# Kernel tuning notes

Hardware: AMD Instinct MI355X
Metric: run time of the kernel (lower is better)

The kernel has to match this reference:

```python
import jax, jax.numpy as jnp
import numpy as np

B, T, C, H = 4, 1024, 1024, 16
D = C // H  # head_dim = 64


def _make_sin_cos(t, d, dtype=jnp.float32):
    # Standard RoPE tables: freqs = pos * inv_freq, emb = concat(freqs, freqs)
    inv_freq = 1.0 / (10000.0 ** (jnp.arange(0, d, 2, dtype=jnp.float32) / d))
    freqs = jnp.arange(t, dtype=jnp.float32)[:, None] * inv_freq[None, :]  # [T, D/2]
    emb = jnp.concatenate([freqs, freqs], axis=-1)  # [T, D]
    return jnp.sin(emb).astype(dtype), jnp.cos(emb).astype(dtype)


def setup_inputs() -> dict:
    key = jax.random.key(0)
    ks = jax.random.split(key, 6)
    sin, cos = _make_sin_cos(T, D)
    return {
        "x": jax.random.normal(ks[0], (B, T, C), jnp.float32),
        "qkv_w": jax.random.normal(ks[1], (3 * C, C), jnp.float32) * (C ** -0.5),
        "qkv_b": jax.random.normal(ks[2], (3 * C,), jnp.float32) * 0.02,
        "out_w": jax.random.normal(ks[3], (C, C), jnp.float32) * (C ** -0.5),
        "out_b": jax.random.normal(ks[4], (C,), jnp.float32) * 0.02,
        "rel_bias": jax.random.normal(ks[5], (H, T, T), jnp.float32) * 0.1,
        "sin": sin,
        "cos": cos,
        "head_gains": jnp.ones((H,), jnp.float32),
    }


def _rotate_half(u):
    u1, u2 = jnp.split(u, 2, axis=-1)
    return jnp.concatenate([-u2, u1], axis=-1)


def reference(x, qkv_w, qkv_b, out_w, out_b, rel_bias, sin, cos, head_gains):
    b, t, c = x.shape
    h, d = H, D
    scale = d ** -0.5
    # QKV projection: [B,T,3C] -> [3,B,H,T,D]
    qkv = (jnp.einsum("btc,oc->bto", x, qkv_w) + qkv_b).reshape(b, t, 3, h, d)
    qkv = jnp.transpose(qkv, (2, 0, 3, 1, 4))
    q, k, v = qkv[0], qkv[1], qkv[2]  # each [B,H,T,D]
    # RoPE
    s = sin[None, None]  # [1,1,T,D]
    co = cos[None, None]
    q = q * co + _rotate_half(q) * s
    k = k * co + _rotate_half(k) * s
    # Scores + additive relative-position bias (non-flash path)
    scores = jnp.einsum("bhtd,bhsd->bhts", q * scale, k) + rel_bias[None]
    attn = jax.nn.softmax(scores, axis=-1)  # dropout_p = 0 (eval)
    ctx = jnp.einsum("bhts,bhsd->bhtd", attn, v)
    ctx = ctx * head_gains[None, :, None, None]  # head-wise gain scaling
    merged = jnp.transpose(ctx, (0, 2, 1, 3)).reshape(b, t, c)
    out = jnp.einsum("btc,oc->bto", merged, out_w) + out_b
    return out, ctx, attn
```

## Files before the change

### kernel.cpp

```cpp
#include <hip/hip_runtime.h>
#include <stdint.h>

#define B_ 4
#define T_ 1024
#define C_ 1024
#define H_ 16
#define D_ 64

typedef __bf16 bf16x8 __attribute__((ext_vector_type(8)));
typedef short  s16x8  __attribute__((ext_vector_type(8)));
typedef short  s16x4  __attribute__((ext_vector_type(4)));
typedef float  f32x4  __attribute__((ext_vector_type(4)));
typedef float  f32x2  __attribute__((ext_vector_type(2)));

__device__ inline f32x4 mfma16(s16x8 a, s16x8 b, f32x4 c) {
    return __builtin_amdgcn_mfma_f32_16x16x32_bf16(a, b, c, 0, 0, 0);
}

__device__ inline void split_pack(f32x4 a, f32x4 b, s16x8& hi, s16x8& lo) {
    bf16x8 h, l;
    #pragma unroll
    for (int j = 0; j < 4; j++) {
        __bf16 x = (__bf16)a[j]; h[j]     = x; l[j]     = (__bf16)(a[j] - (float)x);
        __bf16 y = (__bf16)b[j]; h[j + 4] = y; l[j + 4] = (__bf16)(b[j] - (float)y);
    }
    hi = __builtin_bit_cast(s16x8, h);
    lo = __builtin_bit_cast(s16x8, l);
}

template<int MODE>
__global__ __launch_bounds__(256) void k_gemm_3p(const float* __restrict__ A,
                                                 const float* __restrict__ Bw,
                                                 const float* __restrict__ bias,
                                                 float* __restrict__ Cout,
                                                 int N, int K) {
    const int m0 = blockIdx.y * 128, n0 = blockIdx.x * 128;
    __shared__ __attribute__((aligned(16))) __bf16 Ah[128 * 40];
    __shared__ __attribute__((aligned(16))) __bf16 Al[128 * 40];
    __shared__ __attribute__((aligned(16))) __bf16 Bh[128 * 40];
    __shared__ __attribute__((aligned(16))) __bf16 Bl[128 * 40];
    const int tid = threadIdx.x, lane = tid & 63, wid = tid >> 6;
    const int wm = wid >> 1, wn = wid & 1;
    const int l15 = lane & 15, lh = lane >> 4;
    f32x4 zero = {0.f, 0.f, 0.f, 0.f};
    f32x4 acc[4][4];
    for (int i = 0; i < 4; i++) for (int j = 0; j < 4; j++) acc[i][j] = zero;
    const int r0 = tid >> 2, c8 = (tid & 3) * 8;

    for (int kk = 0; kk < K; kk += 32) {
        __syncthreads();
        #pragma unroll
        for (int g = 0; g < 128; g += 64) {
            int row = m0 + r0 + g;
            const float* ap;
            if (MODE == 0) {
                ap = A + (size_t)row * K + kk + c8;
            } else {
                int b = row >> 10, t = row & 1023;
                int col = kk + c8;
                int h = col >> 6, d = col & 63;
                ap = A + (((size_t)(b * H_ + h) * T_ + t) * D_ + d);
            }
            f32x4 a0 = *(const f32x4*)ap, a1 = *(const f32x4*)(ap + 4);
            s16x8 hi, lo; split_pack(a0, a1, hi, lo);
            *(s16x8*)&Ah[(r0 + g) * 40 + c8] = hi;
            *(s16x8*)&Al[(r0 + g) * 40 + c8] = lo;
            const float* bp = Bw + (size_t)(n0 + r0 + g) * K + kk + c8;
            f32x4 b0 = *(const f32x4*)bp, b1 = *(const f32x4*)(bp + 4);
            s16x8 bhi, blo; split_pack(b0, b1, bhi, blo);
            *(s16x8*)&Bh[(r0 + g) * 40 + c8] = bhi;
            *(s16x8*)&Bl[(r0 + g) * 40 + c8] = blo;
        }
        __syncthreads();
        s16x8 afh[4], afl[4], bfh[4], bfl[4];
        #pragma unroll
        for (int mf = 0; mf < 4; mf++) {
            afh[mf] = *(const s16x8*)&Ah[(wm * 64 + mf * 16 + l15) * 40 + lh * 8];
            afl[mf] = *(const s16x8*)&Al[(wm * 64 + mf * 16 + l15) * 40 + lh * 8];
        }
        #pragma unroll
        for (int nf = 0; nf < 4; nf++) {
            bfh[nf] = *(const s16x8*)&Bh[(wn * 64 + nf * 16 + l15) * 40 + lh * 8];
            bfl[nf] = *(const s16x8*)&Bl[(wn * 64 + nf * 16 + l15) * 40 + lh * 8];
        }
        #pragma unroll
        for (int mf = 0; mf < 4; mf++)
            #pragma unroll
            for (int nf = 0; nf < 4; nf++) {
                acc[mf][nf] = mfma16(afh[mf], bfh[nf], acc[mf][nf]);
                acc[mf][nf] = mfma16(afl[mf], bfh[nf], acc[mf][nf]);
                acc[mf][nf] = mfma16(afh[mf], bfl[nf], acc[mf][nf]);
            }
    }
    #pragma unroll
    for (int mf = 0; mf < 4; mf++)
        #pragma unroll
        for (int nf = 0; nf < 4; nf++)
            #pragma unroll
            for (int r = 0; r < 4; r++) {
                int row = m0 + wm * 64 + mf * 16 + lh * 4 + r;
                int col = n0 + wn * 64 + nf * 16 + l15;
                Cout[(size_t)row * N + col] = acc[mf][nf][r] + bias[col];
            }
}

__global__ __launch_bounds__(256) void k_rope_pack(const float* __restrict__ qkv,
                                                   const float* __restrict__ sinT,
                                                   const float* __restrict__ cosT,
                                                   __bf16* __restrict__ q_hi, __bf16* __restrict__ q_lo,
                                                   __bf16* __restrict__ k_hi, __bf16* __restrict__ k_lo,
                                                   __bf16* __restrict__ v_hi, __bf16* __restrict__ v_lo) {
    const int bh = blockIdx.x >> 4, tc = blockIdx.x & 15;
    const int b = bh >> 4, h = bh & 15;
    const int t0 = tc * 64;
    __shared__ float vt[64 * 72];
    const int tid = threadIdx.x;
    const int tl = tid >> 2, dq = (tid & 3) * 8;
    const int t = t0 + tl;
    const size_t base = ((size_t)(b * T_ + t) * 3) * C_ + h * 64;

    f32x4 s0 = *(const f32x4*)(sinT + t * 64 + dq);
    f32x4 s1 = *(const f32x4*)(sinT + t * 64 + dq + 4);
    f32x4 c0 = *(const f32x4*)(cosT + t * 64 + dq);
    f32x4 c1 = *(const f32x4*)(cosT + t * 64 + dq + 4);

    {
        const int stile = t >> 4, l15t = t & 15;
        const size_t fa0 = (((size_t)(bh * 64 + stile) * 2 + 0) * 64 + (dq >> 3) * 16 + l15t) * 8;
        const size_t fa1 = (((size_t)(bh * 64 + stile) * 2 + 1) * 64 + (dq >> 3) * 16 + l15t) * 8;

        f32x4 ql0 = *(const f32x4*)(qkv + base + dq);
        f32x4 ql1 = *(const f32x4*)(qkv + base + dq + 4);
        f32x4 qu0 = *(const f32x4*)(qkv + base + dq + 32);
        f32x4 qu1 = *(const f32x4*)(qkv + base + dq + 36);
        f32x4 qa0 = (ql0 * c0 - qu0 * s0) * 0.125f;
        f32x4 qa1 = (ql1 * c1 - qu1 * s1) * 0.125f;
        f32x4 qb0 = (qu0 * c0 + ql0 * s0) * 0.125f;
        f32x4 qb1 = (qu1 * c1 + ql1 * s1) * 0.125f;
        s16x8 hi, lo;
        split_pack(qa0, qa1, hi, lo);
        *(s16x8*)(q_hi + fa0) = hi; *(s16x8*)(q_lo + fa0) = lo;
        split_pack(qb0, qb1, hi, lo);
        *(s16x8*)(q_hi + fa1) = hi; *(s16x8*)(q_lo + fa1) = lo;

        f32x4 kl0 = *(const f32x4*)(qkv + base + C_ + dq);
        f32x4 kl1 = *(const f32x4*)(qkv + base + C_ + dq + 4);
        f32x4 ku0 = *(const f32x4*)(qkv + base + C_ + dq + 32);
        f32x4 ku1 = *(const f32x4*)(qkv + base + C_ + dq + 36);
        f32x4 ka0 = kl0 * c0 - ku0 * s0;
        f32x4 ka1 = kl1 * c1 - ku1 * s1;
        f32x4 kb0 = ku0 * c0 + kl0 * s0;
        f32x4 kb1 = ku1 * c1 + kl1 * s1;
        split_pack(ka0, ka1, hi, lo);
        *(s16x8*)(k_hi + fa0) = hi; *(s16x8*)(k_lo + fa0) = lo;
        split_pack(kb0, kb1, hi, lo);
        *(s16x8*)(k_hi + fa1) = hi; *(s16x8*)(k_lo + fa1) = lo;
    }
    {
        f32x4 vl0 = *(const f32x4*)(qkv + base + 2 * C_ + dq);
        f32x4 vl1 = *(const f32x4*)(qkv + base + 2 * C_ + dq + 4);
        f32x4 vu0 = *(const f32x4*)(qkv + base + 2 * C_ + dq + 32);
        f32x4 vu1 = *(const f32x4*)(qkv + base + 2 * C_ + dq + 36);
        #pragma unroll
        for (int j = 0; j < 4; j++) {
            vt[tl * 72 + dq + j]      = vl0[j];
            vt[tl * 72 + dq + 4 + j]  = vl1[j];
            vt[tl * 72 + dq + 32 + j] = vu0[j];
            vt[tl * 72 + dq + 36 + j] = vu1[j];
        }
    }
    __syncthreads();
    const int d = tid >> 2, tq = (tid & 3) * 16;
    bf16x8 h0, h1, l0, l1;
    #pragma unroll
    for (int i = 0; i < 8; i++) {
        float va = vt[(tq + i) * 72 + d];
        float vb = vt[(tq + 8 + i) * 72 + d];
        __bf16 xa = (__bf16)va; h0[i] = xa; l0[i] = (__bf16)(va - (float)xa);
        __bf16 xb = (__bf16)vb; h1[i] = xb; l1[i] = (__bf16)(vb - (float)xb);
    }
    const int s1i = t0 + tq, s2i = s1i + 8;
    const size_t va1 = (((size_t)(bh * 32 + (s1i >> 5)) * 4 + (d >> 4)) * 64 +
                       ((s1i & 31) >> 3) * 16 + (d & 15)) * 8;
    const size_t va2 = (((size_t)(bh * 32 + (s2i >> 5)) * 4 + (d >> 4)) * 64 +
                       ((s2i & 31) >> 3) * 16 + (d & 15)) * 8;
    *(s16x8*)(v_hi + va1) = __builtin_bit_cast(s16x8, h0);
    *(s16x8*)(v_hi + va2) = __builtin_bit_cast(s16x8, h1);
    *(s16x8*)(v_lo + va1) = __builtin_bit_cast(s16x8, l0);
    *(s16x8*)(v_lo + va2) = __builtin_bit_cast(s16x8, l1);
}

#define PB_PITCH 1048
__global__ __launch_bounds__(512, 4) void k_fused(const __bf16* __restrict__ q_hi, const __bf16* __restrict__ q_lo,
                                                  const __bf16* __restrict__ k_hi, const __bf16* __restrict__ k_lo,
                                                  const __bf16* __restrict__ v_hi, const __bf16* __restrict__ v_lo,
                                                  const float* __restrict__ rel_bias,
                                                  const float* __restrict__ gains,
                                                  float* __restrict__ attn_out,
                                                  float* __restrict__ ctx_out) {
    const int wg = (blockIdx.x & 7) * 512 + (blockIdx.x >> 3);
    const int bh = wg >> 6, t0 = (wg & 63) * 16;
    const int h = bh & 15;
    __shared__ __attribute__((aligned(16))) __bf16 Pb[16 * PB_PITCH];
    __shared__ float red_m[16][9];
    __shared__ float red_s[16][9];
    float* sc2 = (float*)Pb;
    const int tid = threadIdx.x, lane = tid & 63, w = tid >> 6;
    const int l15 = lane & 15, lh = lane >> 4;
    f32x4 zero = {0.f, 0.f, 0.f, 0.f};

    {
        const int row = tid >> 5, lane32 = tid & 31;
        const float* br = rel_bias + ((size_t)h * T_ + t0 + row) * T_;
        #pragma unroll
        for (int kk = 0; kk < 8; kk++) {
            int col = kk * 128 + lane32 * 4;
            f32x4 bv = *(const f32x4*)(br + col);
            s16x4 p;
            p[0] = __builtin_bit_cast(short, (__bf16)bv[0]);
            p[1] = __builtin_bit_cast(short, (__bf16)bv[1]);
            p[2] = __builtin_bit_cast(short, (__bf16)bv[2]);
            p[3] = __builtin_bit_cast(short, (__bf16)bv[3]);
            *(s16x4*)&Pb[row * PB_PITCH + col] = p;
        }
    }

    s16x8 aq0h, aq0l, aq1h, aq1l;
    {
        const __bf16* qb = q_hi + (size_t)(bh * 64 + (t0 >> 4)) * 1024;
        const __bf16* ql = q_lo + (size_t)(bh * 64 + (t0 >> 4)) * 1024;
        aq0h = *(const s16x8*)(qb + lane * 8);
        aq1h = *(const s16x8*)(qb + 512 + lane * 8);
        aq0l = *(const s16x8*)(ql + lane * 8);
        aq1l = *(const s16x8*)(ql + 512 + lane * 8);
    }
    f32x4 acc[8];
    #pragma unroll
    for (int i = 0; i < 8; i++) acc[i] = zero;
    #pragma unroll
    for (int nf = 0; nf < 8; nf++) {
        const size_t kb = (size_t)(bh * 64 + w * 8 + nf) * 1024;
        s16x8 kh0 = *(const s16x8*)(k_hi + kb + lane * 8);
        s16x8 kh1 = *(const s16x8*)(k_hi + kb + 512 + lane * 8);
        s16x8 kl0 = *(const s16x8*)(k_lo + kb + lane * 8);
        s16x8 kl1 = *(const s16x8*)(k_lo + kb + 512 + lane * 8);
        acc[nf] = mfma16(aq0h, kh0, acc[nf]);
        acc[nf] = mfma16(aq0l, kh0, acc[nf]);
        acc[nf] = mfma16(aq0h, kl0, acc[nf]);
        acc[nf] = mfma16(aq1h, kh1, acc[nf]);
        acc[nf] = mfma16(aq1l, kh1, acc[nf]);
        acc[nf] = mfma16(aq1h, kl1, acc[nf]);
    }
    __syncthreads();
    #pragma unroll
    for (int nf = 0; nf < 8; nf++)
        #pragma unroll
        for (int r = 0; r < 4; r++)
            acc[nf][r] += (float)Pb[(lh * 4 + r) * PB_PITCH + w * 128 + nf * 16 + l15];

    float m[4];
    #pragma unroll
    for (int r = 0; r < 4; r++) {
        float mm = acc[0][r];
        #pragma unroll
        for (int nf = 1; nf < 8; nf++) mm = fmaxf(mm, acc[nf][r]);
        m[r] = mm;
    }
    #pragma unroll
    for (int o = 8; o >= 1; o >>= 1)
        #pragma unroll
        for (int r = 0; r < 4; r++) m[r] = fmaxf(m[r], __shfl_xor(m[r], o));
    if (l15 == 0) {
        #pragma unroll
        for (int r = 0; r < 4; r++) red_m[lh * 4 + r][w] = m[r];
    }
    __syncthreads();
    #pragma unroll
    for (int r = 0; r < 4; r++) {
        float mm = red_m[lh * 4 + r][0];
        #pragma unroll
        for (int w2 = 1; w2 < 8; w2++) mm = fmaxf(mm, red_m[lh * 4 + r][w2]);
        m[r] = mm;
    }
    float s[4] = {0.f, 0.f, 0.f, 0.f};
    #pragma unroll
    for (int nf = 0; nf < 8; nf++)
        #pragma unroll
        for (int r = 0; r < 4; r++) {
            float e = __expf(acc[nf][r] - m[r]);
            acc[nf][r] = e;
            s[r] += e;
        }
    #pragma unroll
    for (int o = 8; o >= 1; o >>= 1)
        #pragma unroll
        for (int r = 0; r < 4; r++) s[r] += __shfl_xor(s[r], o);
    if (l15 == 0) {
        #pragma unroll
        for (int r = 0; r < 4; r++) red_s[lh * 4 + r][w] = s[r];
    }
    __syncthreads();
    float inv[4];
    #pragma unroll
    for (int r = 0; r < 4; r++) {
        float ss = red_s[lh * 4 + r][0];
        #pragma unroll
        for (int w2 = 1; w2 < 8; w2++) ss += red_s[lh * 4 + r][w2];
        inv[r] = 1.f / ss;
    }
    #pragma unroll
    for (int nf = 0; nf < 8; nf++)
        #pragma unroll
        for (int r = 0; r < 4; r++)
            Pb[(lh * 4 + r) * PB_PITCH + w * 128 + nf * 16 + l15] =
                (__bf16)(acc[nf][r] * inv[r]);
    __syncthreads();

    {
        const int row = 2 * w + (lane >> 5);
        const int cg = lane & 31;
        float* arow = attn_out + ((size_t)bh * T_ + t0 + row) * T_;
        #pragma unroll
        for (int p = 0; p < 4; p++) {
            int col = p * 256 + cg * 8;
            bf16x8 pv8 = *(const bf16x8*)&Pb[row * PB_PITCH + col];
            f32x4 lo4 = {(float)pv8[0], (float)pv8[1], (float)pv8[2], (float)pv8[3]};
            f32x4 hi4 = {(float)pv8[4], (float)pv8[5], (float)pv8[6], (float)pv8[7]};
            *(f32x4*)(arow + col)     = lo4;
            *(f32x4*)(arow + col + 4) = hi4;
        }
    }

    f32x4 cacc[4];
    #pragma unroll
    for (int i = 0; i < 4; i++) cacc[i] = zero;
    #pragma unroll
    for (int ks = 0; ks < 4; ks++) {
        int sbase = w * 128 + ks * 32;
        s16x8 pa = __builtin_bit_cast(s16x8,
                   *(const bf16x8*)&Pb[l15 * PB_PITCH + sbase + lh * 8]);
        #pragma unroll
        for (int nf = 0; nf < 4; nf++) {
            const size_t vb = (size_t)((bh * 32 + w * 4 + ks) * 4 + nf) * 512;
            s16x8 vh = *(const s16x8*)(v_hi + vb + lane * 8);
            s16x8 vl = *(const s16x8*)(v_lo + vb + lane * 8);
            cacc[nf] = mfma16(pa, vh, cacc[nf]);
            cacc[nf] = mfma16(pa, vl, cacc[nf]);
        }
    }
    __syncthreads();
    #pragma unroll
    for (int nf = 0; nf < 4; nf++)
        #pragma unroll
        for (int r = 0; r < 4; r++)
            sc2[w * 1024 + (lh * 4 + r) * 64 + nf * 16 + l15] = cacc[nf][r];
    __syncthreads();
    {
        int e0 = tid * 2;
        int crow = e0 >> 6, d = e0 & 63;
        f32x2 sm = *(const f32x2*)&sc2[e0];
        #pragma unroll
        for (int w2 = 1; w2 < 8; w2++) sm += *(const f32x2*)&sc2[w2 * 1024 + e0];
        float g = gains[h];
        sm[0] *= g; sm[1] *= g;
        *(f32x2*)(ctx_out + ((size_t)bh * T_ + t0 + crow) * 64 + d) = sm;
    }
}

extern "C" void kernel_launch(void* const* d_in, const int* in_sizes, int n_in,
                              void* d_out, int out_size, void* d_ws, size_t ws_size,
                              hipStream_t stream) {
    const float* x        = (const float*)d_in[0];
    const float* qkv_w    = (const float*)d_in[1];
    const float* qkv_b    = (const float*)d_in[2];
    const float* out_w    = (const float*)d_in[3];
    const float* out_b    = (const float*)d_in[4];
    const float* rel_bias = (const float*)d_in[5];
    const float* sinT     = (const float*)d_in[6];
    const float* cosT     = (const float*)d_in[7];
    const float* gains    = (const float*)d_in[8];

    float* out  = (float*)d_out;
    float* ctx  = out + (size_t)B_ * T_ * C_;
    float* attn = ctx + (size_t)B_ * H_ * T_ * D_;

    char* ws = (char*)d_ws;
    __bf16* q_hi = (__bf16*)(ws);
    __bf16* q_lo = (__bf16*)(ws + ((size_t)8 << 20));
    __bf16* k_hi = (__bf16*)(ws + ((size_t)16 << 20));
    __bf16* k_lo = (__bf16*)(ws + ((size_t)24 << 20));
    __bf16* v_hi = (__bf16*)(ws + ((size_t)32 << 20));
    __bf16* v_lo = (__bf16*)(ws + ((size_t)40 << 20));
    float* qkvF = attn;

    k_gemm_3p<0><<<dim3(24, 32), 256, 0, stream>>>(x, qkv_w, qkv_b, qkvF, 3072, 1024);
    k_rope_pack<<<1024, 256, 0, stream>>>(qkvF, sinT, cosT, q_hi, q_lo, k_hi, k_lo, v_hi, v_lo);
    k_fused<<<4096, 512, 0, stream>>>(q_hi, q_lo, k_hi, k_lo, v_hi, v_lo,
                                      rel_bias, gains, attn, ctx);
    k_gemm_3p<1><<<dim3(8, 32), 256, 0, stream>>>(ctx, out_w, out_b, out, 1024, 1024);
}
```

Before: 367.7 us.

## Batch K loads, merge softmax reductions into one barrier, prefetch V fragments

The QK^T loop now issues all eight K-fragment loads per half before the MFMAs, which exposes more memory-level parallelism. The softmax computes local max and sum per wave and combines them with an online-softmax rescale, so one of the block-wide syncs is removed. V fragments are double-buffered in registers and prefetched ahead of the PV MFMAs, with the first batch issued before the attn write-out. These changes raise register pressure, which may reduce occupancy.

```diff
diff --git a/kernel.cpp b/kernel.cpp
--- a/kernel.cpp
+++ b/kernel.cpp
@@ -237,19 +237,32 @@
     f32x4 acc[8];
     #pragma unroll
     for (int i = 0; i < 8; i++) acc[i] = zero;
-    #pragma unroll
-    for (int nf = 0; nf < 8; nf++) {
-        const size_t kb = (size_t)(bh * 64 + w * 8 + nf) * 1024;
-        s16x8 kh0 = *(const s16x8*)(k_hi + kb + lane * 8);
-        s16x8 kh1 = *(const s16x8*)(k_hi + kb + 512 + lane * 8);
-        s16x8 kl0 = *(const s16x8*)(k_lo + kb + lane * 8);
-        s16x8 kl1 = *(const s16x8*)(k_lo + kb + 512 + lane * 8);
-        acc[nf] = mfma16(aq0h, kh0, acc[nf]);
-        acc[nf] = mfma16(aq0l, kh0, acc[nf]);
-        acc[nf] = mfma16(aq0h, kl0, acc[nf]);
-        acc[nf] = mfma16(aq1h, kh1, acc[nf]);
-        acc[nf] = mfma16(aq1l, kh1, acc[nf]);
-        acc[nf] = mfma16(aq1h, kl1, acc[nf]);
+    {
+        s16x8 kfh[8], kfl[8];
+        #pragma unroll
+        for (int nf = 0; nf < 8; nf++) {
+            const size_t kb = (size_t)(bh * 64 + w * 8 + nf) * 1024;
+            kfh[nf] = *(const s16x8*)(k_hi + kb + lane * 8);
+            kfl[nf] = *(const s16x8*)(k_lo + kb + lane * 8);
+        }
+        #pragma unroll
+        for (int nf = 0; nf < 8; nf++) {
+            acc[nf] = mfma16(aq0h, kfh[nf], acc[nf]);
+            acc[nf] = mfma16(aq0l, kfh[nf], acc[nf]);
+            acc[nf] = mfma16(aq0h, kfl[nf], acc[nf]);
+        }
+        #pragma unroll
+        for (int nf = 0; nf < 8; nf++) {
+            const size_t kb = (size_t)(bh * 64 + w * 8 + nf) * 1024 + 512;
+            kfh[nf] = *(const s16x8*)(k_hi + kb + lane * 8);
+            kfl[nf] = *(const s16x8*)(k_lo + kb + lane * 8);
+        }
+        #pragma unroll
+        for (int nf = 0; nf < 8; nf++) {
+            acc[nf] = mfma16(aq1h, kfh[nf], acc[nf]);
+            acc[nf] = mfma16(aq1l, kfh[nf], acc[nf]);
+            acc[nf] = mfma16(aq1h, kfl[nf], acc[nf]);
+        }
     }
     __syncthreads();
     #pragma unroll
@@ -258,7 +271,7 @@
         for (int r = 0; r < 4; r++)
             acc[nf][r] += (float)Pb[(lh * 4 + r) * PB_PITCH + w * 128 + nf * 16 + l15];
 
-    float m[4];
+    float m[4], s[4];
     #pragma unroll
     for (int r = 0; r < 4; r++) {
         float mm = acc[0][r];
@@ -270,19 +283,8 @@
     for (int o = 8; o >= 1; o >>= 1)
         #pragma unroll
         for (int r = 0; r < 4; r++) m[r] = fmaxf(m[r], __shfl_xor(m[r], o));
-    if (l15 == 0) {
-        #pragma unroll
-        for (int r = 0; r < 4; r++) red_m[lh * 4 + r][w] = m[r];
-    }
-    __syncthreads();
-    #pragma unroll
-    for (int r = 0; r < 4; r++) {
-        float mm = red_m[lh * 4 + r][0];
-        #pragma unroll
-        for (int w2 = 1; w2 < 8; w2++) mm = fmaxf(mm, red_m[lh * 4 + r][w2]);
-        m[r] = mm;
-    }
-    float s[4] = {0.f, 0.f, 0.f, 0.f};
+    #pragma unroll
+    for (int r = 0; r < 4; r++) s[r] = 0.f;
     #pragma unroll
     for (int nf = 0; nf < 8; nf++)
         #pragma unroll
@@ -297,24 +299,40 @@
         for (int r = 0; r < 4; r++) s[r] += __shfl_xor(s[r], o);
     if (l15 == 0) {
         #pragma unroll
-        for (int r = 0; r < 4; r++) red_s[lh * 4 + r][w] = s[r];
-    }
-    __syncthreads();
-    float inv[4];
+        for (int r = 0; r < 4; r++) {
+            red_m[lh * 4 + r][w] = m[r];
+            red_s[lh * 4 + r][w] = s[r];
+        }
+    }
+    __syncthreads();
+    float fac[4];
     #pragma unroll
     for (int r = 0; r < 4; r++) {
-        float ss = red_s[lh * 4 + r][0];
-        #pragma unroll
-        for (int w2 = 1; w2 < 8; w2++) ss += red_s[lh * 4 + r][w2];
-        inv[r] = 1.f / ss;
+        int row = lh * 4 + r;
+        float M = red_m[row][0];
+        #pragma unroll
+        for (int w2 = 1; w2 < 8; w2++) M = fmaxf(M, red_m[row][w2]);
+        float S = 0.f;
+        #pragma unroll
+        for (int w2 = 0; w2 < 8; w2++)
+            S += red_s[row][w2] * __expf(red_m[row][w2] - M);
+        fac[r] = __expf(m[r] - M) / S;
     }
     #pragma unroll
     for (int nf = 0; nf < 8; nf++)
         #pragma unroll
         for (int r = 0; r < 4; r++)
             Pb[(lh * 4 + r) * PB_PITCH + w * 128 + nf * 16 + l15] =
-                (__bf16)(acc[nf][r] * inv[r]);
-    __syncthreads();
+                (__bf16)(acc[nf][r] * fac[r]);
+    __syncthreads();
+
+    s16x8 vh[2][4], vl[2][4];
+    #pragma unroll
+    for (int nf = 0; nf < 4; nf++) {
+        const size_t vb = (size_t)((bh * 32 + w * 4 + 0) * 4 + nf) * 512;
+        vh[0][nf] = *(const s16x8*)(v_hi + vb + lane * 8);
+        vl[0][nf] = *(const s16x8*)(v_lo + vb + lane * 8);
+    }
 
     {
         const int row = 2 * w + (lane >> 5);
@@ -336,16 +354,22 @@
     for (int i = 0; i < 4; i++) cacc[i] = zero;
     #pragma unroll
     for (int ks = 0; ks < 4; ks++) {
+        const int cur = ks & 1, nxt = cur ^ 1;
+        if (ks < 3) {
+            #pragma unroll
+            for (int nf = 0; nf < 4; nf++) {
+                const size_t vb = (size_t)((bh * 32 + w * 4 + ks + 1) * 4 + nf) * 512;
+                vh[nxt][nf] = *(const s16x8*)(v_hi + vb + lane * 8);
+                vl[nxt][nf] = *(const s16x8*)(v_lo + vb + lane * 8);
+            }
+        }
         int sbase = w * 128 + ks * 32;
         s16x8 pa = __builtin_bit_cast(s16x8,
                    *(const bf16x8*)&Pb[l15 * PB_PITCH + sbase + lh * 8]);
         #pragma unroll
         for (int nf = 0; nf < 4; nf++) {
-            const size_t vb = (size_t)((bh * 32 + w * 4 + ks) * 4 + nf) * 512;
-            s16x8 vh = *(const s16x8*)(v_hi + vb + lane * 8);
-            s16x8 vl = *(const s16x8*)(v_lo + vb + lane * 8);
-            cacc[nf] = mfma16(pa, vh, cacc[nf]);
-            cacc[nf] = mfma16(pa, vl, cacc[nf]);
+            cacc[nf] = mfma16(pa, vh[cur][nf], cacc[nf]);
+            cacc[nf] = mfma16(pa, vl[cur][nf], cacc[nf]);
         }
     }
     __syncthreads();
```

Result: no change. 367.1 us (-0.2%).

## Process 32 query rows per block and merge softmax max/sum reductions

Applied to the files above, without the earlier changes.

Each attention block now handles two 16-row query tiles instead of one, so every K and V fragment loaded from global memory feeds twice as many MFMAs, and the grid halves. The separate max and sum cross-wave reductions are combined into one pass that rescales each wave's partial sums by exp(local max - global max), removing a block-wide barrier. In exchange, LDS use per block doubles (32-row Pb plus larger reduction arrays) and register pressure rises, which can lower occupancy under the 512x4 launch bounds.

```diff
diff --git a/kernel.cpp b/kernel.cpp
--- a/kernel.cpp
+++ b/kernel.cpp
@@ -198,23 +198,23 @@
                                                   const float* __restrict__ gains,
                                                   float* __restrict__ attn_out,
                                                   float* __restrict__ ctx_out) {
-    const int wg = (blockIdx.x & 7) * 512 + (blockIdx.x >> 3);
-    const int bh = wg >> 6, t0 = (wg & 63) * 16;
+    const int wg = (blockIdx.x & 7) * 256 + (blockIdx.x >> 3);
+    const int bh = wg >> 5, t0 = (wg & 31) * 32;
     const int h = bh & 15;
-    __shared__ __attribute__((aligned(16))) __bf16 Pb[16 * PB_PITCH];
-    __shared__ float red_m[16][9];
-    __shared__ float red_s[16][9];
+    __shared__ __attribute__((aligned(16))) __bf16 Pb[32 * PB_PITCH];
+    __shared__ float red_m[32][9];
+    __shared__ float red_s[32][9];
     float* sc2 = (float*)Pb;
     const int tid = threadIdx.x, lane = tid & 63, w = tid >> 6;
     const int l15 = lane & 15, lh = lane >> 4;
     f32x4 zero = {0.f, 0.f, 0.f, 0.f};
 
     {
-        const int row = tid >> 5, lane32 = tid & 31;
+        const int row = tid >> 4, lane16 = tid & 15;
         const float* br = rel_bias + ((size_t)h * T_ + t0 + row) * T_;
         #pragma unroll
-        for (int kk = 0; kk < 8; kk++) {
-            int col = kk * 128 + lane32 * 4;
+        for (int kk = 0; kk < 16; kk++) {
+            int col = kk * 64 + lane16 * 4;
             f32x4 bv = *(const f32x4*)(br + col);
             s16x4 p;
             p[0] = __builtin_bit_cast(short, (__bf16)bv[0]);
@@ -225,18 +225,21 @@
         }
     }
 
-    s16x8 aq0h, aq0l, aq1h, aq1l;
-    {
-        const __bf16* qb = q_hi + (size_t)(bh * 64 + (t0 >> 4)) * 1024;
-        const __bf16* ql = q_lo + (size_t)(bh * 64 + (t0 >> 4)) * 1024;
-        aq0h = *(const s16x8*)(qb + lane * 8);
-        aq1h = *(const s16x8*)(qb + 512 + lane * 8);
-        aq0l = *(const s16x8*)(ql + lane * 8);
-        aq1l = *(const s16x8*)(ql + 512 + lane * 8);
-    }
-    f32x4 acc[8];
-    #pragma unroll
-    for (int i = 0; i < 8; i++) acc[i] = zero;
+    s16x8 aqh[2][2], aql[2][2];
+    #pragma unroll
+    for (int tt = 0; tt < 2; tt++) {
+        const __bf16* qb = q_hi + (size_t)(bh * 64 + (t0 >> 4) + tt) * 1024;
+        const __bf16* ql = q_lo + (size_t)(bh * 64 + (t0 >> 4) + tt) * 1024;
+        aqh[tt][0] = *(const s16x8*)(qb + lane * 8);
+        aqh[tt][1] = *(const s16x8*)(qb + 512 + lane * 8);
+        aql[tt][0] = *(const s16x8*)(ql + lane * 8);
+        aql[tt][1] = *(const s16x8*)(ql + 512 + lane * 8);
+    }
+    f32x4 acc[2][8];
+    #pragma unroll
+    for (int tt = 0; tt < 2; tt++)
+        #pragma unroll
+        for (int i = 0; i < 8; i++) acc[tt][i] = zero;
     #pragma unroll
     for (int nf = 0; nf < 8; nf++) {
         const size_t kb = (size_t)(bh * 64 + w * 8 + nf) * 1024;
@@ -244,80 +247,100 @@
         s16x8 kh1 = *(const s16x8*)(k_hi + kb + 512 + lane * 8);
         s16x8 kl0 = *(const s16x8*)(k_lo + kb + lane * 8);
         s16x8 kl1 = *(const s16x8*)(k_lo + kb + 512 + lane * 8);
-        acc[nf] = mfma16(aq0h, kh0, acc[nf]);
-        acc[nf] = mfma16(aq0l, kh0, acc[nf]);
-        acc[nf] = mfma16(aq0h, kl0, acc[nf]);
-        acc[nf] = mfma16(aq1h, kh1, acc[nf]);
-        acc[nf] = mfma16(aq1l, kh1, acc[nf]);
-        acc[nf] = mfma16(aq1h, kl1, acc[nf]);
-    }
-    __syncthreads();
-    #pragma unroll
-    for (int nf = 0; nf < 8; nf++)
-        #pragma unroll
-        for (int r = 0; r < 4; r++)
-            acc[nf][r] += (float)Pb[(lh * 4 + r) * PB_PITCH + w * 128 + nf * 16 + l15];
-
-    float m[4];
-    #pragma unroll
-    for (int r = 0; r < 4; r++) {
-        float mm = acc[0][r];
-        #pragma unroll
-        for (int nf = 1; nf < 8; nf++) mm = fmaxf(mm, acc[nf][r]);
-        m[r] = mm;
-    }
+        #pragma unroll
+        for (int tt = 0; tt < 2; tt++) {
+            acc[tt][nf] = mfma16(aqh[tt][0], kh0, acc[tt][nf]);
+            acc[tt][nf] = mfma16(aql[tt][0], kh0, acc[tt][nf]);
+            acc[tt][nf] = mfma16(aqh[tt][0], kl0, acc[tt][nf]);
+            acc[tt][nf] = mfma16(aqh[tt][1], kh1, acc[tt][nf]);
+            acc[tt][nf] = mfma16(aql[tt][1], kh1, acc[tt][nf]);
+            acc[tt][nf] = mfma16(aqh[tt][1], kl1, acc[tt][nf]);
+        }
+    }
+    __syncthreads();
+    #pragma unroll
+    for (int tt = 0; tt < 2; tt++)
+        #pragma unroll
+        for (int nf = 0; nf < 8; nf++)
+            #pragma unroll
+            for (int r = 0; r < 4; r++)
+                acc[tt][nf][r] +=
+                    (float)Pb[(tt * 16 + lh * 4 + r) * PB_PITCH + w * 128 + nf * 16 + l15];
+
+    float m[2][4], s[2][4];
+    #pragma unroll
+    for (int tt = 0; tt < 2; tt++)
+        #pragma unroll
+        for (int r = 0; r < 4; r++) {
+            float mm = acc[tt][0][r];
+            #pragma unroll
+            for (int nf = 1; nf < 8; nf++) mm = fmaxf(mm, acc[tt][nf][r]);
+            m[tt][r] = mm;
+        }
     #pragma unroll
     for (int o = 8; o >= 1; o >>= 1)
         #pragma unroll
-        for (int r = 0; r < 4; r++) m[r] = fmaxf(m[r], __shfl_xor(m[r], o));
+        for (int tt = 0; tt < 2; tt++)
+            #pragma unroll
+            for (int r = 0; r < 4; r++) m[tt][r] = fmaxf(m[tt][r], __shfl_xor(m[tt][r], o));
+    #pragma unroll
+    for (int tt = 0; tt < 2; tt++)
+        #pragma unroll
+        for (int r = 0; r < 4; r++) s[tt][r] = 0.f;
+    #pragma unroll
+    for (int tt = 0; tt < 2; tt++)
+        #pragma unroll
+        for (int nf = 0; nf < 8; nf++)
+            #pragma unroll
+            for (int r = 0; r < 4; r++) {
+                float e = __expf(acc[tt][nf][r] - m[tt][r]);
+                acc[tt][nf][r] = e;
+                s[tt][r] += e;
+            }
+    #pragma unroll
+    for (int o = 8; o >= 1; o >>= 1)
+        #pragma unroll
+        for (int tt = 0; tt < 2; tt++)
+            #pragma unroll
+            for (int r = 0; r < 4; r++) s[tt][r] += __shfl_xor(s[tt][r], o);
     if (l15 == 0) {
         #pragma unroll
-        for (int r = 0; r < 4; r++) red_m[lh * 4 + r][w] = m[r];
-    }
-    __syncthreads();
-    #pragma unroll
-    for (int r = 0; r < 4; r++) {
-        float mm = red_m[lh * 4 + r][0];
-        #pragma unroll
-        for (int w2 = 1; w2 < 8; w2++) mm = fmaxf(mm, red_m[lh * 4 + r][w2]);
-        m[r] = mm;
-    }
-    float s[4] = {0.f, 0.f, 0.f, 0.f};
-    #pragma unroll
-    for (int nf = 0; nf < 8; nf++)
+        for (int tt = 0; tt < 2; tt++)
+            #pragma unroll
+            for (int r = 0; r < 4; r++) {
+                red_m[tt * 16 + lh * 4 + r][w] = m[tt][r];
+                red_s[tt * 16 + lh * 4 + r][w] = s[tt][r];
+            }
+    }
+    __syncthreads();
+    float fac[2][4];
+    #pragma unroll
+    for (int tt = 0; tt < 2; tt++)
         #pragma unroll
         for (int r = 0; r < 4; r++) {
-            float e = __expf(acc[nf][r] - m[r]);
-            acc[nf][r] = e;
-            s[r] += e;
-        }
-    #pragma unroll
-    for (int o = 8; o >= 1; o >>= 1)
-        #pragma unroll
-        for (int r = 0; r < 4; r++) s[r] += __shfl_xor(s[r], o);
-    if (l15 == 0) {
-        #pragma unroll
-        for (int r = 0; r < 4; r++) red_s[lh * 4 + r][w] = s[r];
-    }
-    __syncthreads();
-    float inv[4];
-    #pragma unroll
-    for (int r = 0; r < 4; r++) {
-        float ss = red_s[lh * 4 + r][0];
-        #pragma unroll
-        for (int w2 = 1; w2 < 8; w2++) ss += red_s[lh * 4 + r][w2];
-        inv[r] = 1.f / ss;
-    }
-    #pragma unroll
-    for (int nf = 0; nf < 8; nf++)
-        #pragma unroll
-        for (int r = 0; r < 4; r++)
-            Pb[(lh * 4 + r) * PB_PITCH + w * 128 + nf * 16 + l15] =
-                (__bf16)(acc[nf][r] * inv[r]);
-    __syncthreads();
-
-    {
-        const int row = 2 * w + (lane >> 5);
+            int row = tt * 16 + lh * 4 + r;
+            float M = red_m[row][0];
+            #pragma unroll
+            for (int w2 = 1; w2 < 8; w2++) M = fmaxf(M, red_m[row][w2]);
+            float S = 0.f;
+            #pragma unroll
+            for (int w2 = 0; w2 < 8; w2++)
+                S += red_s[row][w2] * __expf(red_m[row][w2] - M);
+            fac[tt][r] = __expf(m[tt][r] - M) / S;
+        }
+    #pragma unroll
+    for (int tt = 0; tt < 2; tt++)
+        #pragma unroll
+        for (int nf = 0; nf < 8; nf++)
+            #pragma unroll
+            for (int r = 0; r < 4; r++)
+                Pb[(tt * 16 + lh * 4 + r) * PB_PITCH + w * 128 + nf * 16 + l15] =
+                    (__bf16)(acc[tt][nf][r] * fac[tt][r]);
+    __syncthreads();
+
+    #pragma unroll
+    for (int rp = 0; rp < 2; rp++) {
+        const int row = 4 * w + 2 * rp + (lane >> 5);
         const int cg = lane & 31;
         float* arow = attn_out + ((size_t)bh * T_ + t0 + row) * T_;
         #pragma unroll
@@ -331,39 +354,50 @@
         }
     }
 
-    f32x4 cacc[4];
-    #pragma unroll
-    for (int i = 0; i < 4; i++) cacc[i] = zero;
+    f32x4 cacc[2][4];
+    #pragma unroll
+    for (int tt = 0; tt < 2; tt++)
+        #pragma unroll
+        for (int i = 0; i < 4; i++) cacc[tt][i] = zero;
     #pragma unroll
     for (int ks = 0; ks < 4; ks++) {
         int sbase = w * 128 + ks * 32;
-        s16x8 pa = __builtin_bit_cast(s16x8,
-                   *(const bf16x8*)&Pb[l15 * PB_PITCH + sbase + lh * 8]);
+        s16x8 pa[2];
+        #pragma unroll
+        for (int tt = 0; tt < 2; tt++)
+            pa[tt] = __builtin_bit_cast(s16x8,
+                     *(const bf16x8*)&Pb[(tt * 16 + l15) * PB_PITCH + sbase + lh * 8]);
         #pragma unroll
         for (int nf = 0; nf < 4; nf++) {
             const size_t vb = (size_t)((bh * 32 + w * 4 + ks) * 4 + nf) * 512;
             s16x8 vh = *(const s16x8*)(v_hi + vb + lane * 8);
             s16x8 vl = *(const s16x8*)(v_lo + vb + lane * 8);
-            cacc[nf] = mfma16(pa, vh, cacc[nf]);
-            cacc[nf] = mfma16(pa, vl, cacc[nf]);
-        }
-    }
-    __syncthreads();
-    #pragma unroll
-    for (int nf = 0; nf < 4; nf++)
-        #pragma unroll
-        for (int r = 0; r < 4; r++)
-            sc2[w * 1024 + (lh * 4 + r) * 64 + nf * 16 + l15] = cacc[nf][r];
+            #pragma unroll
+            for (int tt = 0; tt < 2; tt++) {
+                cacc[tt][nf] = mfma16(pa[tt], vh, cacc[tt][nf]);
+                cacc[tt][nf] = mfma16(pa[tt], vl, cacc[tt][nf]);
+            }
+        }
+    }
+    __syncthreads();
+    #pragma unroll
+    for (int tt = 0; tt < 2; tt++)
+        #pragma unroll
+        for (int nf = 0; nf < 4; nf++)
+            #pragma unroll
+            for (int r = 0; r < 4; r++)
+                sc2[tt * 8192 + w * 1024 + (lh * 4 + r) * 64 + nf * 16 + l15] = cacc[tt][nf][r];
     __syncthreads();
     {
-        int e0 = tid * 2;
-        int crow = e0 >> 6, d = e0 & 63;
-        f32x2 sm = *(const f32x2*)&sc2[e0];
-        #pragma unroll
-        for (int w2 = 1; w2 < 8; w2++) sm += *(const f32x2*)&sc2[w2 * 1024 + e0];
+        int e0 = tid * 4;
+        int tt = e0 >> 10, rem = e0 & 1023;
+        int crow = rem >> 6, d = rem & 63;
+        f32x4 sm = *(const f32x4*)&sc2[tt * 8192 + rem];
+        #pragma unroll
+        for (int w2 = 1; w2 < 8; w2++) sm += *(const f32x4*)&sc2[tt * 8192 + w2 * 1024 + rem];
         float g = gains[h];
-        sm[0] *= g; sm[1] *= g;
-        *(f32x2*)(ctx_out + ((size_t)bh * T_ + t0 + crow) * 64 + d) = sm;
+        sm *= g;
+        *(f32x4*)(ctx_out + ((size_t)bh * T_ + t0 + tt * 16 + crow) * 64 + d) = sm;
     }
 }
 
@@ -395,7 +429,7 @@
 
     k_gemm_3p<0><<<dim3(24, 32), 256, 0, stream>>>(x, qkv_w, qkv_b, qkvF, 3072, 1024);
     k_rope_pack<<<1024, 256, 0, stream>>>(qkvF, sinT, cosT, q_hi, q_lo, k_hi, k_lo, v_hi, v_lo);
-    k_fused<<<4096, 512, 0, stream>>>(q_hi, q_lo, k_hi, k_lo, v_hi, v_lo,
+    k_fused<<<2048, 512, 0, stream>>>(q_hi, q_lo, k_hi, k_lo, v_hi, v_lo,
                                       rel_bias, gains, attn, ctx);
     k_gemm_3p<1><<<dim3(8, 32), 256, 0, stream>>>(ctx, out_w, out_b, out, 1024, 1024);
 }
```

New measurement: 367.3 us. No clear change (-0.1%).

## Reuse rel_bias tile across batch loop and merge softmax reductions

Applied to the files above, without the earlier changes.

Each workgroup now handles one (head, 16-row) tile for all 4 batches, staging the rel_bias tile in shared memory once and reusing it for every batch, so bias reads from global memory drop by a factor of four. The grid shrinks from 4096 to 1024 blocks. Softmax max and sum reductions are merged into a single barrier with an online-softmax style rescale across waves. The cost is more shared memory per block, which may lower occupancy, fewer blocks for latency hiding, and serialised batches within a block.

```diff
diff --git a/kernel.cpp b/kernel.cpp
--- a/kernel.cpp
+++ b/kernel.cpp
@@ -191,6 +191,7 @@
 }
 
 #define PB_PITCH 1048
+#define BL_PITCH 1028
 __global__ __launch_bounds__(512, 4) void k_fused(const __bf16* __restrict__ q_hi, const __bf16* __restrict__ q_lo,
                                                   const __bf16* __restrict__ k_hi, const __bf16* __restrict__ k_lo,
                                                   const __bf16* __restrict__ v_hi, const __bf16* __restrict__ v_lo,
@@ -198,9 +199,9 @@
                                                   const float* __restrict__ gains,
                                                   float* __restrict__ attn_out,
                                                   float* __restrict__ ctx_out) {
-    const int wg = (blockIdx.x & 7) * 512 + (blockIdx.x >> 3);
-    const int bh = wg >> 6, t0 = (wg & 63) * 16;
-    const int h = bh & 15;
+    const int wg = (blockIdx.x & 7) * 128 + (blockIdx.x >> 3);
+    const int h = wg >> 6, t0 = (wg & 63) * 16;
+    __shared__ __attribute__((aligned(16))) __bf16 BiasL[16 * BL_PITCH];
     __shared__ __attribute__((aligned(16))) __bf16 Pb[16 * PB_PITCH];
     __shared__ float red_m[16][9];
     __shared__ float red_s[16][9];
@@ -208,6 +209,7 @@
     const int tid = threadIdx.x, lane = tid & 63, w = tid >> 6;
     const int l15 = lane & 15, lh = lane >> 4;
     f32x4 zero = {0.f, 0.f, 0.f, 0.f};
+    const float g = gains[h];
 
     {
         const int row = tid >> 5, lane32 = tid & 31;
@@ -221,149 +223,149 @@
             p[1] = __builtin_bit_cast(short, (__bf16)bv[1]);
             p[2] = __builtin_bit_cast(short, (__bf16)bv[2]);
             p[3] = __builtin_bit_cast(short, (__bf16)bv[3]);
-            *(s16x4*)&Pb[row * PB_PITCH + col] = p;
-        }
-    }
-
-    s16x8 aq0h, aq0l, aq1h, aq1l;
-    {
-        const __bf16* qb = q_hi + (size_t)(bh * 64 + (t0 >> 4)) * 1024;
-        const __bf16* ql = q_lo + (size_t)(bh * 64 + (t0 >> 4)) * 1024;
-        aq0h = *(const s16x8*)(qb + lane * 8);
-        aq1h = *(const s16x8*)(qb + 512 + lane * 8);
-        aq0l = *(const s16x8*)(ql + lane * 8);
-        aq1l = *(const s16x8*)(ql + 512 + lane * 8);
-    }
-    f32x4 acc[8];
-    #pragma unroll
-    for (int i = 0; i < 8; i++) acc[i] = zero;
-    #pragma unroll
-    for (int nf = 0; nf < 8; nf++) {
-        const size_t kb = (size_t)(bh * 64 + w * 8 + nf) * 1024;
-        s16x8 kh0 = *(const s16x8*)(k_hi + kb + lane * 8);
-        s16x8 kh1 = *(const s16x8*)(k_hi + kb + 512 + lane * 8);
-        s16x8 kl0 = *(const s16x8*)(k_lo + kb + lane * 8);
-        s16x8 kl1 = *(const s16x8*)(k_lo + kb + 512 + lane * 8);
-        acc[nf] = mfma16(aq0h, kh0, acc[nf]);
-        acc[nf] = mfma16(aq0l, kh0, acc[nf]);
-        acc[nf] = mfma16(aq0h, kl0, acc[nf]);
-        acc[nf] = mfma16(aq1h, kh1, acc[nf]);
-        acc[nf] = mfma16(aq1l, kh1, acc[nf]);
-        acc[nf] = mfma16(aq1h, kl1, acc[nf]);
+            *(s16x4*)&BiasL[row * BL_PITCH + col] = p;
+        }
     }
     __syncthreads();
-    #pragma unroll
-    for (int nf = 0; nf < 8; nf++)
-        #pragma unroll
-        for (int r = 0; r < 4; r++)
-            acc[nf][r] += (float)Pb[(lh * 4 + r) * PB_PITCH + w * 128 + nf * 16 + l15];
-
-    float m[4];
-    #pragma unroll
-    for (int r = 0; r < 4; r++) {
-        float mm = acc[0][r];
-        #pragma unroll
-        for (int nf = 1; nf < 8; nf++) mm = fmaxf(mm, acc[nf][r]);
-        m[r] = mm;
-    }
-    #pragma unroll
-    for (int o = 8; o >= 1; o >>= 1)
-        #pragma unroll
-        for (int r = 0; r < 4; r++) m[r] = fmaxf(m[r], __shfl_xor(m[r], o));
-    if (l15 == 0) {
-        #pragma unroll
-        for (int r = 0; r < 4; r++) red_m[lh * 4 + r][w] = m[r];
-    }
-    __syncthreads();
-    #pragma unroll
-    for (int r = 0; r < 4; r++) {
-        float mm = red_m[lh * 4 + r][0];
-        #pragma unroll
-        for (int w2 = 1; w2 < 8; w2++) mm = fmaxf(mm, red_m[lh * 4 + r][w2]);
-        m[r] = mm;
-    }
-    float s[4] = {0.f, 0.f, 0.f, 0.f};
-    #pragma unroll
-    for (int nf = 0; nf < 8; nf++)
+
+    for (int b = 0; b < 4; b++) {
+        const int bh = b * H_ + h;
+
+        s16x8 aq0h, aq0l, aq1h, aq1l;
+        {
+            const __bf16* qb = q_hi + (size_t)(bh * 64 + (t0 >> 4)) * 1024;
+            const __bf16* ql = q_lo + (size_t)(bh * 64 + (t0 >> 4)) * 1024;
+            aq0h = *(const s16x8*)(qb + lane * 8);
+            aq1h = *(const s16x8*)(qb + 512 + lane * 8);
+            aq0l = *(const s16x8*)(ql + lane * 8);
+            aq1l = *(const s16x8*)(ql + 512 + lane * 8);
+        }
+        f32x4 acc[8];
+        #pragma unroll
+        for (int i = 0; i < 8; i++) acc[i] = zero;
+        #pragma unroll
+        for (int nf = 0; nf < 8; nf++) {
+            const size_t kb = (size_t)(bh * 64 + w * 8 + nf) * 1024;
+            s16x8 kh0 = *(const s16x8*)(k_hi + kb + lane * 8);
+            s16x8 kh1 = *(const s16x8*)(k_hi + kb + 512 + lane * 8);
+            s16x8 kl0 = *(const s16x8*)(k_lo + kb + lane * 8);
+            s16x8 kl1 = *(const s16x8*)(k_lo + kb + 512 + lane * 8);
+            acc[nf] = mfma16(aq0h, kh0, acc[nf]);
+            acc[nf] = mfma16(aq0l, kh0, acc[nf]);
+            acc[nf] = mfma16(aq0h, kl0, acc[nf]);
+            acc[nf] = mfma16(aq1h, kh1, acc[nf]);
+            acc[nf] = mfma16(aq1l, kh1, acc[nf]);
+            acc[nf] = mfma16(aq1h, kl1, acc[nf]);
+        }
+        #pragma unroll
+        for (int nf = 0; nf < 8; nf++)
+            #pragma unroll
+            for (int r = 0; r < 4; r++)
+                acc[nf][r] += (float)BiasL[(lh * 4 + r) * BL_PITCH + w * 128 + nf * 16 + l15];
+
+        float m[4], s[4];
         #pragma unroll
         for (int r = 0; r < 4; r++) {
-            float e = __expf(acc[nf][r] - m[r]);
-            acc[nf][r] = e;
-            s[r] += e;
-        }
-    #pragma unroll
-    for (int o = 8; o >= 1; o >>= 1)
-        #pragma unroll
-        for (int r = 0; r < 4; r++) s[r] += __shfl_xor(s[r], o);
-    if (l15 == 0) {
-        #pragma unroll
-        for (int r = 0; r < 4; r++) red_s[lh * 4 + r][w] = s[r];
-    }
-    __syncthreads();
-    float inv[4];
-    #pragma unroll
-    for (int r = 0; r < 4; r++) {
-        float ss = red_s[lh * 4 + r][0];
-        #pragma unroll
-        for (int w2 = 1; w2 < 8; w2++) ss += red_s[lh * 4 + r][w2];
-        inv[r] = 1.f / ss;
-    }
-    #pragma unroll
-    for (int nf = 0; nf < 8; nf++)
-        #pragma unroll
-        for (int r = 0; r < 4; r++)
-            Pb[(lh * 4 + r) * PB_PITCH + w * 128 + nf * 16 + l15] =
-                (__bf16)(acc[nf][r] * inv[r]);
-    __syncthreads();
-
-    {
-        const int row = 2 * w + (lane >> 5);
-        const int cg = lane & 31;
-        float* arow = attn_out + ((size_t)bh * T_ + t0 + row) * T_;
-        #pragma unroll
-        for (int p = 0; p < 4; p++) {
-            int col = p * 256 + cg * 8;
-            bf16x8 pv8 = *(const bf16x8*)&Pb[row * PB_PITCH + col];
-            f32x4 lo4 = {(float)pv8[0], (float)pv8[1], (float)pv8[2], (float)pv8[3]};
-            f32x4 hi4 = {(float)pv8[4], (float)pv8[5], (float)pv8[6], (float)pv8[7]};
-            *(f32x4*)(arow + col)     = lo4;
-            *(f32x4*)(arow + col + 4) = hi4;
-        }
-    }
-
-    f32x4 cacc[4];
-    #pragma unroll
-    for (int i = 0; i < 4; i++) cacc[i] = zero;
-    #pragma unroll
-    for (int ks = 0; ks < 4; ks++) {
-        int sbase = w * 128 + ks * 32;
-        s16x8 pa = __builtin_bit_cast(s16x8,
-                   *(const bf16x8*)&Pb[l15 * PB_PITCH + sbase + lh * 8]);
-        #pragma unroll
-        for (int nf = 0; nf < 4; nf++) {
-            const size_t vb = (size_t)((bh * 32 + w * 4 + ks) * 4 + nf) * 512;
-            s16x8 vh = *(const s16x8*)(v_hi + vb + lane * 8);
-            s16x8 vl = *(const s16x8*)(v_lo + vb + lane * 8);
-            cacc[nf] = mfma16(pa, vh, cacc[nf]);
-            cacc[nf] = mfma16(pa, vl, cacc[nf]);
-        }
-    }
-    __syncthreads();
-    #pragma unroll
-    for (int nf = 0; nf < 4; nf++)
-        #pragma unroll
-        for (int r = 0; r < 4; r++)
-            sc2[w * 1024 + (lh * 4 + r) * 64 + nf * 16 + l15] = cacc[nf][r];
-    __syncthreads();
-    {
-        int e0 = tid * 2;
-        int crow = e0 >> 6, d = e0 & 63;
-        f32x2 sm = *(const f32x2*)&sc2[e0];
-        #pragma unroll
-        for (int w2 = 1; w2 < 8; w2++) sm += *(const f32x2*)&sc2[w2 * 1024 + e0];
-        float g = gains[h];
-        sm[0] *= g; sm[1] *= g;
-        *(f32x2*)(ctx_out + ((size_t)bh * T_ + t0 + crow) * 64 + d) = sm;
+            float mm = acc[0][r];
+            #pragma unroll
+            for (int nf = 1; nf < 8; nf++) mm = fmaxf(mm, acc[nf][r]);
+            m[r] = mm;
+        }
+        #pragma unroll
+        for (int o = 8; o >= 1; o >>= 1)
+            #pragma unroll
+            for (int r = 0; r < 4; r++) m[r] = fmaxf(m[r], __shfl_xor(m[r], o));
+        #pragma unroll
+        for (int r = 0; r < 4; r++) s[r] = 0.f;
+        #pragma unroll
+        for (int nf = 0; nf < 8; nf++)
+            #pragma unroll
+            for (int r = 0; r < 4; r++) {
+                float e = __expf(acc[nf][r] - m[r]);
+                acc[nf][r] = e;
+                s[r] += e;
+            }
+        #pragma unroll
+        for (int o = 8; o >= 1; o >>= 1)
+            #pragma unroll
+            for (int r = 0; r < 4; r++) s[r] += __shfl_xor(s[r], o);
+        if (l15 == 0) {
+            #pragma unroll
+            for (int r = 0; r < 4; r++) {
+                red_m[lh * 4 + r][w] = m[r];
+                red_s[lh * 4 + r][w] = s[r];
+            }
+        }
+        __syncthreads();
+        float fac[4];
+        #pragma unroll
+        for (int r = 0; r < 4; r++) {
+            int row = lh * 4 + r;
+            float M = red_m[row][0];
+            #pragma unroll
+            for (int w2 = 1; w2 < 8; w2++) M = fmaxf(M, red_m[row][w2]);
+            float S = 0.f;
+            #pragma unroll
+            for (int w2 = 0; w2 < 8; w2++)
+                S += red_s[row][w2] * __expf(red_m[row][w2] - M);
+            fac[r] = __expf(m[r] - M) / S;
+        }
+        #pragma unroll
+        for (int nf = 0; nf < 8; nf++)
+            #pragma unroll
+            for (int r = 0; r < 4; r++)
+                Pb[(lh * 4 + r) * PB_PITCH + w * 128 + nf * 16 + l15] =
+                    (__bf16)(acc[nf][r] * fac[r]);
+        __syncthreads();
+
+        {
+            const int row = 2 * w + (lane >> 5);
+            const int cg = lane & 31;
+            float* arow = attn_out + ((size_t)bh * T_ + t0 + row) * T_;
+            #pragma unroll
+            for (int p = 0; p < 4; p++) {
+                int col = p * 256 + cg * 8;
+                bf16x8 pv8 = *(const bf16x8*)&Pb[row * PB_PITCH + col];
+                f32x4 lo4 = {(float)pv8[0], (float)pv8[1], (float)pv8[2], (float)pv8[3]};
+                f32x4 hi4 = {(float)pv8[4], (float)pv8[5], (float)pv8[6], (float)pv8[7]};
+                *(f32x4*)(arow + col)     = lo4;
+                *(f32x4*)(arow + col + 4) = hi4;
+            }
+        }
+
+        f32x4 cacc[4];
+        #pragma unroll
+        for (int i = 0; i < 4; i++) cacc[i] = zero;
+        #pragma unroll
+        for (int ks = 0; ks < 4; ks++) {
+            int sbase = w * 128 + ks * 32;
+            s16x8 pa = __builtin_bit_cast(s16x8,
+                       *(const bf16x8*)&Pb[l15 * PB_PITCH + sbase + lh * 8]);
+            #pragma unroll
+            for (int nf = 0; nf < 4; nf++) {
+                const size_t vb = (size_t)((bh * 32 + w * 4 + ks) * 4 + nf) * 512;
+                s16x8 vh = *(const s16x8*)(v_hi + vb + lane * 8);
+                s16x8 vl = *(const s16x8*)(v_lo + vb + lane * 8);
+                cacc[nf] = mfma16(pa, vh, cacc[nf]);
+                cacc[nf] = mfma16(pa, vl, cacc[nf]);
+            }
+        }
+        __syncthreads();
+        #pragma unroll
+        for (int nf = 0; nf < 4; nf++)
+            #pragma unroll
+            for (int r = 0; r < 4; r++)
+                sc2[w * 1024 + (lh * 4 + r) * 64 + nf * 16 + l15] = cacc[nf][r];
+        __syncthreads();
+        {
+            int e0 = tid * 2;
+            int crow = e0 >> 6, d = e0 & 63;
+            f32x2 sm = *(const f32x2*)&sc2[e0];
+            #pragma unroll
+            for (int w2 = 1; w2 < 8; w2++) sm += *(const f32x2*)&sc2[w2 * 1024 + e0];
+            sm[0] *= g; sm[1] *= g;
+            *(f32x2*)(ctx_out + ((size_t)bh * T_ + t0 + crow) * 64 + d) = sm;
+        }
     }
 }
 
@@ -395,7 +397,7 @@
 
     k_gemm_3p<0><<<dim3(24, 32), 256, 0, stream>>>(x, qkv_w, qkv_b, qkvF, 3072, 1024);
     k_rope_pack<<<1024, 256, 0, stream>>>(qkvF, sinT, cosT, q_hi, q_lo, k_hi, k_lo, v_hi, v_lo);
-    k_fused<<<4096, 512, 0, stream>>>(q_hi, q_lo, k_hi, k_lo, v_hi, v_lo,
+    k_fused<<<1024, 512, 0, stream>>>(q_hi, q_lo, k_hi, k_lo, v_hi, v_lo,
                                       rel_bias, gains, attn, ctx);
     k_gemm_3p<1><<<dim3(8, 32), 256, 0, stream>>>(ctx, out_w, out_b, out, 1024, 1024);
 }
```

New measurement: 333.8 us. 1.1x faster.
